# Kernel optimization log

Measured on AMD Instinct MI355X. Metric: run time of the kernel, lower is better.

Reference implementation:

```python
import jax, jax.numpy as jnp
import numpy as np

B, N, PLANE, H, W = 2, 6, 64, 48, 48
HIDP = 64
PS = 3
RATES = 3


def conv2d(x, w, b, pad, dil=1):
    # x: [BN, Cin, H, W], w: [Cout, Cin, kh, kw]
    out = jax.lax.conv_general_dilated(
        x, w, window_strides=(1, 1),
        padding=[(pad, pad), (pad, pad)],
        rhs_dilation=(dil, dil),
        dimension_numbers=('NCHW', 'OIHW', 'NCHW'))
    return out + b[None, :, None, None]


def avgpool3(x):
    bn, c, h, w = x.shape
    return x.reshape(bn, c, h // PS, PS, w // PS, PS).mean(axis=(3, 5))


def setup_inputs() -> dict:
    key = jax.random.key(0)
    ks = jax.random.split(key, 20)
    s = 0.05
    hid_pa = PLANE * 3  # 192, hidden width of MultiFieldConv2d
    d = {
        'x': jax.random.normal(ks[0], (B, N, PLANE, H, W), jnp.float32),
        # patch_aggr: 3 dilated convs (rates 1..3), k=3, plane -> plane*3
        'pa_w1': jax.random.normal(ks[1], (hid_pa, PLANE, 3, 3)) * s,
        'pa_b1': jnp.zeros((hid_pa,)),
        'pa_w2': jax.random.normal(ks[2], (hid_pa, PLANE, 3, 3)) * s,
        'pa_b2': jnp.zeros((hid_pa,)),
        'pa_w3': jax.random.normal(ks[3], (hid_pa, PLANE, 3, 3)) * s,
        'pa_b3': jnp.zeros((hid_pa,)),
        # convert: 1x1 (hid_pa*rates -> 3*hidp), relu, 1x1 (3*hidp -> 3*hidp)
        'pa_cw1': jax.random.normal(ks[4], (3 * HIDP, hid_pa * RATES, 1, 1)) * s,
        'pa_cb1': jnp.zeros((3 * HIDP,)),
        'pa_cw2': jax.random.normal(ks[5], (3 * HIDP, 3 * HIDP, 1, 1)) * s,
        'pa_cb2': jnp.zeros((3 * HIDP,)),
        # to_kv conv: k=3 pad=1, hidp -> hidp
        'kv_w': jax.random.normal(ks[6], (HIDP, HIDP, 3, 3)) * s,
        'kv_b': jnp.zeros((HIDP,)),
        # to_out: 1x1 hidp->plane, relu, 1x1 plane->plane, relu
        'out_w1': jax.random.normal(ks[7], (PLANE, HIDP, 1, 1)) * s,
        'out_b1': jnp.zeros((PLANE,)),
        'out_w2': jax.random.normal(ks[8], (PLANE, PLANE, 1, 1)) * s,
        'out_b2': jnp.zeros((PLANE,)),
        'scales': jnp.ones((N,)),
    }
    return d


def reference(x, pa_w1, pa_b1, pa_w2, pa_b2, pa_w3, pa_b3,
              pa_cw1, pa_cb1, pa_cw2, pa_cb2,
              kv_w, kv_b, out_w1, out_b1, out_w2, out_b2, scales):
    b, n, c, h, w = x.shape
    scale = HIDP ** (-0.5)
    xf = x.reshape(b * n, c, h, w)

    # MultiFieldConv2d: dilated convs (same spatial size for odd k), concat, 1x1 convert
    u = jnp.concatenate([
        conv2d(xf, pa_w1, pa_b1, pad=1, dil=1),
        conv2d(xf, pa_w2, pa_b2, pad=2, dil=2),
        conv2d(xf, pa_w3, pa_b3, pad=3, dil=3),
    ], axis=1)
    qkv = conv2d(jax.nn.relu(conv2d(u, pa_cw1, pa_cb1, 0)), pa_cw2, pa_cb2, 0)
    qkv = jax.nn.relu(qkv)  # F.relu(patch_aggr(x))
    xq, xk, xv = jnp.split(qkv, 3, axis=1)  # each [BN, hidp, H, W]

    def to_kv(t):
        return avgpool3(jax.nn.relu(conv2d(t, kv_w, kv_b, pad=PS // 2)))

    k_ = to_kv(xk)                       # [BN, hidp, H/3, W/3]
    v_ = to_kv(xv) * (1.0 / PS ** 2)

    hw_kv = k_.shape[2] * k_.shape[3]
    Qs = xq.reshape(b, n, HIDP, h * w).transpose(0, 1, 3, 2)   # b n g d
    Ks = k_.reshape(b, n, HIDP, hw_kv).transpose(0, 1, 3, 2)   # b m k d
    Vs = v_.reshape(b, n, HIDP, hw_kv).transpose(0, 1, 3, 2)

    # Leave-one-out sigmoid attention: sum_{j != i} sigmoid(q_i k_j^T * scale) @ v_j
    # Computed as full sum minus the self (j == i) term (exact same math).
    A_all = jax.nn.sigmoid(jnp.einsum('bngd,bmkd->bngmk', Qs, Ks) * scale)
    out_all = jnp.einsum('bngmk,bmkd->bngd', A_all, Vs)
    A_self = jax.nn.sigmoid(jnp.einsum('bngd,bnkd->bngk', Qs, Ks) * scale)
    out_self = jnp.einsum('bngk,bnkd->bngd', A_self, Vs)
    attn_out = out_all - out_self                               # [b, n, HW, hidp]

    res = attn_out.transpose(0, 1, 3, 2).reshape(b, n, HIDP, h, w)
    xv5 = xv.reshape(b, n, HIDP, h, w)
    res = jax.nn.relu(res + scales[None, :, None, None, None] * xv5)

    rf = res.reshape(b * n, HIDP, h, w)
    o = jax.nn.relu(conv2d(jax.nn.relu(conv2d(rf, out_w1, out_b1, 0)), out_w2, out_b2, 0))
    return o.reshape(b, n, c, h, w)
```

## Files before the change

kernel.cpp:

```cpp
#include <hip/hip_runtime.h>
#include <hip/hip_bf16.h>
#include <math.h>

#define BB 2
#define NVIEW 6
#define BN 12
#define CIN 64
#define HH 48
#define WW 48
#define PP (HH*WW)
#define OC 192
#define HPA 192
#define HIDP 64
#define KHW 16
#define PK 256
#define PADW 54
#define PADA (PADW*PADW)
#define NTOT (BN*PP)
#define K1 1728
#define KVPW 50
#define KVPA (KVPW*KVPW)

typedef __attribute__((ext_vector_type(8))) short bf16x8;
typedef __attribute__((ext_vector_type(4))) float f32x4;

#define OFF_WEFFB 0
#define SZ_WEFFB_FL (OC*K1/2)
#define OFF_BEFF (OFF_WEFFB + SZ_WEFFB_FL)
#define SZ_BEFF 256
#define OFF_CW2B (OFF_BEFF + SZ_BEFF)
#define SZ_CW2B_FL (OC*OC/2)
#define OFF_WKVB (OFF_CW2B + SZ_CW2B_FL)
#define SZ_WKVB_FL (64*576/2)
#define OFF_PADXT (OFF_WKVB + SZ_WKVB_FL)
#define SZ_PADXT_FL (BN*PADA*64/2)
#define OFF_QB16 (OFF_PADXT + SZ_PADXT_FL)
#define SZ_QB16_FL (BN*PP*64/2)
#define OFF_KB16 (OFF_QB16 + SZ_QB16_FL)
#define SZ_KB16_FL (BN*PK*64/2)
#define OFF_VB16T (OFF_KB16 + SZ_KB16_FL)
#define SZ_VB16T_FL (BN*64*PK/2)
#define OFF_KVPAD (OFF_VB16T + SZ_VB16T_FL)
#define SZ_KVPAD_FL (BN*2*KVPA*64/2)
#define OFF_CONVB (OFF_KVPAD + SZ_KVPAD_FL)
#define SZ_CONVB_FL (BN*2*PP*64/2)
#define OFF_W1SW (OFF_CONVB + SZ_CONVB_FL)
#define SZ_WSW_FL 2048
#define OFF_W2SW (OFF_W1SW + SZ_WSW_FL)
#define OFF_ATTNP (OFF_W2SW + SZ_WSW_FL)
#define SZ_ATTNP (BN*PP*HIDP)
#define OFF_XVB16 (OFF_ATTNP + 2*SZ_ATTNP)
#define SZ_XVB16_FL (BN*PP*64/2)

__device__ __forceinline__ void load_lds16(const void* g, void* l) {
    __builtin_amdgcn_global_load_lds(
        (const __attribute__((address_space(1))) unsigned int*)g,
        (__attribute__((address_space(3))) unsigned int*)l, 16, 0, 0);
}

__device__ __forceinline__ unsigned short f2bu(float f) {
    __hip_bfloat16 h = __float2bfloat16(f);
    return *(unsigned short*)&h;
}

__device__ __forceinline__ float bu2f(unsigned short h) {
    unsigned int u = ((unsigned int)h) << 16;
    return *(float*)&u;
}

__global__ void k_fold(const float* __restrict__ cw1, const float* __restrict__ cb1,
                       const float* __restrict__ w1, const float* __restrict__ b1,
                       const float* __restrict__ w2, const float* __restrict__ b2,
                       const float* __restrict__ w3, const float* __restrict__ b3,
                       __hip_bfloat16* __restrict__ weffb, float* __restrict__ beff) {
    int r = blockIdx.x / OC;
    int o = blockIdx.x % OC;
    int t = threadIdx.x;
    int ic = t / 9, tap = t % 9;
    const float* w = (r==0) ? w1 : (r==1) ? w2 : w3;
    float acc = 0.f;
    for (int c = 0; c < HPA; ++c)
        acc += cw1[o*(HPA*3) + r*HPA + c] * w[c*(CIN*9) + t];
    weffb[(size_t)o*K1 + r*576 + tap*64 + ic] = __float2bfloat16(acc);
    if (r == 0 && t == 0) {
        float bacc = cb1[o];
        for (int rr = 0; rr < 3; ++rr) {
            const float* bb = (rr==0)?b1:(rr==1)?b2:b3;
            for (int c = 0; c < HPA; ++c)
                bacc += cw1[o*(HPA*3) + rr*HPA + c] * bb[c];
        }
        beff[o] = bacc;
    }
}

__global__ void k_wprep(const float* __restrict__ kvw, const float* __restrict__ cw2,
                        const float* __restrict__ w1, const float* __restrict__ w2,
                        __hip_bfloat16* __restrict__ wkvb, __hip_bfloat16* __restrict__ cw2b,
                        __hip_bfloat16* __restrict__ w1sw, __hip_bfloat16* __restrict__ w2sw) {
    int idx = blockIdx.x*256 + threadIdx.x;
    if (idx < 36864) {
        int oc = idx / 576, rest = idx % 576;
        int tap = rest / 64, ic = rest % 64;
        wkvb[idx] = __float2bfloat16(kvw[(oc*64 + ic)*9 + tap]);
    } else if (idx < 73728) {
        int i = idx - 36864;
        cw2b[i] = __float2bfloat16(cw2[i]);
    } else if (idx < 81920) {
        int i = idx - 73728;
        const float* w = (i < 4096) ? w1 : w2;
        __hip_bfloat16* dst = (i < 4096) ? w1sw : w2sw;
        int j = i & 4095;
        int oc = j >> 6, s = (j >> 3) & 7, e = j & 7;
        int k = ((s ^ (oc & 7)) << 3) + e;
        dst[j] = __float2bfloat16(w[oc*64 + k]);
    }
}

__global__ void k_padxT(const float* __restrict__ x, __hip_bfloat16* __restrict__ padxT) {
    int idx = blockIdx.x*256 + threadIdx.x;
    if (idx >= BN*PADA) return;
    int spos = idx % PADA; int bn = idx / PADA;
    int sy = spos / PADW, sx = spos % PADW;
    __hip_bfloat16* dst = padxT + (size_t)idx*64;
    if (sy >= 3 && sy < 51 && sx >= 3 && sx < 51) {
        const float* src = x + (size_t)bn*CIN*PP + (sy-3)*WW + (sx-3);
        #pragma unroll 8
        for (int ic = 0; ic < 64; ++ic) dst[ic] = __float2bfloat16(src[ic*PP]);
    } else {
        #pragma unroll 8
        for (int ic = 0; ic < 64; ++ic) dst[ic] = __float2bfloat16(0.f);
    }
}

__global__ void k_zero(__hip_bfloat16* __restrict__ kvpad) {
    size_t idx = ((size_t)blockIdx.x*256 + threadIdx.x)*8;
    bf16x8 z = (bf16x8){0,0,0,0,0,0,0,0};
    *(bf16x8*)(kvpad + idx) = z;
}

__global__ __launch_bounds__(512) void k_mfc(const __hip_bfloat16* __restrict__ wA,
        const __hip_bfloat16* __restrict__ pxT, const __hip_bfloat16* __restrict__ cw2b,
        const float* __restrict__ beff, const float* __restrict__ cb2,
        __hip_bfloat16* __restrict__ xvb16, __hip_bfloat16* __restrict__ qb16,
        __hip_bfloat16* __restrict__ kvpad) {
    __shared__ __align__(16) char smem[58368];
    int tid = threadIdx.x;
    int wid = tid >> 6, lane = tid & 63;
    int bn = blockIdx.x / 18;
    int pb = (blockIdx.x % 18) * 128;
    int sgr = ((lane&7) ^ (lane>>3)) * 8;
    int wr = wid >> 1, wc = wid & 1;
    int l7 = lane & 7, lh = lane >> 4, rrow = lane & 15, gcol = lane >> 4;

    size_t gbase[5];
    #pragma unroll
    for (int s2 = 0; s2 < 5; ++s2) {
        int seg = wid*5 + s2;
        if (seg < 24) {
            int row = seg*8 + (lane>>3);
            gbase[s2] = (size_t)row*K1 + sgr;
        } else {
            int p = pb + (seg-24)*8 + (lane>>3);
            int py = p / WW, px = p % WW;
            gbase[s2] = ((size_t)bn*PADA + (py+3)*PADW + (px+3))*64 + sgr;
        }
    }

    f32x4 acc1[3][4];
    #pragma unroll
    for (int m = 0; m < 3; ++m)
        #pragma unroll
        for (int nf = 0; nf < 4; ++nf) acc1[m][nf] = (f32x4){0.f,0.f,0.f,0.f};

    for (int kt = 0; kt < 27; ++kt) {
        int r_ = kt / 9, tap = kt - r_*9;
        int doff = (r_+1)*((tap/3 - 1)*PADW + (tap%3 - 1));
        __syncthreads();
        #pragma unroll
        for (int s2 = 0; s2 < 5; ++s2) {
            int seg = wid*5 + s2;
            const __hip_bfloat16* g = (seg < 24) ? wA + gbase[s2] + kt*64
                                                 : pxT + gbase[s2] + (size_t)doff*64;
            load_lds16(g, smem + seg*1024);
        }
        __syncthreads();
        bf16x8 a[3][2], b[4][2];
        #pragma unroll
        for (int kk = 0; kk < 2; ++kk) {
            int gof = ((kk*4 + lh) ^ l7) << 4;
            #pragma unroll
            for (int m = 0; m < 3; ++m)
                a[m][kk] = *(const bf16x8*)(smem + (wr*48 + m*16 + rrow)*128 + gof);
            #pragma unroll
            for (int nf = 0; nf < 4; ++nf)
                b[nf][kk] = *(const bf16x8*)(smem + 24576 + (wc*64 + nf*16 + rrow)*128 + gof);
        }
        #pragma unroll
        for (int kk = 0; kk < 2; ++kk)
            #pragma unroll
            for (int m = 0; m < 3; ++m)
                #pragma unroll
                for (int nf = 0; nf < 4; ++nf)
                    acc1[m][nf] = __builtin_amdgcn_mfma_f32_16x16x32_bf16(
                        a[m][kk], b[nf][kk], acc1[m][nf], 0, 0, 0);
    }

    f32x4 acc2[3][4];
    #pragma unroll
    for (int m = 0; m < 3; ++m)
        #pragma unroll
        for (int nf = 0; nf < 4; ++nf) acc2[m][nf] = (f32x4){0.f,0.f,0.f,0.f};

    for (int kt2 = 0; kt2 < 3; ++kt2) {
        __syncthreads();
        #pragma unroll
        for (int s2 = 0; s2 < 3; ++s2) {
            int seg = wid*3 + s2;
            int row = seg*8 + (lane>>3);
            load_lds16(cw2b + (size_t)row*OC + kt2*64 + sgr, smem + seg*1024);
        }
        #pragma unroll
        for (int m = 0; m < 3; ++m) {
            int oc16 = wr*48 + m*16;
            if ((oc16 >> 6) == kt2) {
                int oc0 = oc16 + gcol*4;
                float4 bz = *(const float4*)&beff[oc0];
                int cb = (oc0 - kt2*64)*2;
                #pragma unroll
                for (int nf = 0; nf < 4; ++nf) {
                    int px = wc*64 + nf*16 + rrow;
                    ushort4 hv;
                    hv.x = f2bu(fmaxf(acc1[m][nf][0] + bz.x, 0.f));
                    hv.y = f2bu(fmaxf(acc1[m][nf][1] + bz.y, 0.f));
                    hv.z = f2bu(fmaxf(acc1[m][nf][2] + bz.z, 0.f));
                    hv.w = f2bu(fmaxf(acc1[m][nf][3] + bz.w, 0.f));
                    *(ushort4*)(smem + 40960 + px*136 + cb) = hv;
                }
            }
        }
        __syncthreads();
        #pragma unroll
        for (int kk = 0; kk < 2; ++kk) {
            int gofA = ((kk*4 + lh) ^ l7) << 4;
            int gofB = (kk*4 + lh) << 4;
            bf16x8 a2[3], b2[4];
            #pragma unroll
            for (int m2 = 0; m2 < 3; ++m2)
                a2[m2] = *(const bf16x8*)(smem + (wr*48 + m2*16 + rrow)*128 + gofA);
            #pragma unroll
            for (int nf = 0; nf < 4; ++nf)
                b2[nf] = *(const bf16x8*)(smem + 40960 + (wc*64 + nf*16 + rrow)*136 + gofB);
            #pragma unroll
            for (int m2 = 0; m2 < 3; ++m2)
                #pragma unroll
                for (int nf = 0; nf < 4; ++nf)
                    acc2[m2][nf] = __builtin_amdgcn_mfma_f32_16x16x32_bf16(
                        a2[m2], b2[nf], acc2[m2][nf], 0, 0, 0);
        }
    }

    #pragma unroll
    for (int m2 = 0; m2 < 3; ++m2) {
        int oc16 = wr*48 + m2*16;
        int sec = oc16 >> 6;
        int oc0 = oc16 + gcol*4;
        float4 cz = *(const float4*)&cb2[oc0];
        #pragma unroll
        for (int nf = 0; nf < 4; ++nf) {
            int px = wc*64 + nf*16 + rrow;
            int p = pb + px;
            ushort4 bv;
            bv.x = f2bu(fmaxf(acc2[m2][nf][0] + cz.x, 0.f));
            bv.y = f2bu(fmaxf(acc2[m2][nf][1] + cz.y, 0.f));
            bv.z = f2bu(fmaxf(acc2[m2][nf][2] + cz.z, 0.f));
            bv.w = f2bu(fmaxf(acc2[m2][nf][3] + cz.w, 0.f));
            if (sec == 0) {
                *(ushort4*)&qb16[((size_t)bn*PP + p)*64 + oc0] = bv;
            } else {
                int kv = sec - 1;
                int py = p / WW, pxx = p % WW;
                int d = oc0 - (sec << 6);
                *(ushort4*)&kvpad[((size_t)(bn*2+kv)*KVPA + (py+1)*KVPW + pxx+1)*64 + d] = bv;
                if (kv == 1)
                    *(ushort4*)&xvb16[((size_t)bn*PP + p)*64 + d] = bv;
            }
        }
    }
}

__global__ __launch_bounds__(256) void k_kvgemm(const __hip_bfloat16* __restrict__ wA,
        const __hip_bfloat16* __restrict__ kvpad, const float* __restrict__ kvb,
        __hip_bfloat16* __restrict__ convb) {
    __shared__ __align__(16) char smem[24576];
    int tid = threadIdx.x;
    int wid = tid >> 6, lane = tid & 63;
    int tileN = blockIdx.x * 128;
    int bn2 = tileN / PP, p0 = tileN % PP;
    int sgr = ((lane&7) ^ (lane>>3)) * 8;

    size_t gbase[6];
    #pragma unroll
    for (int s2 = 0; s2 < 6; ++s2) {
        int seg = wid*6 + s2;
        if (seg < 8) {
            int row = seg*8 + (lane>>3);
            gbase[s2] = (size_t)row*576 + sgr;
        } else {
            int p = p0 + (seg-8)*8 + (lane>>3);
            int py = p / WW, px = p % WW;
            gbase[s2] = ((size_t)bn2*KVPA + (py+1)*KVPW + px+1)*64 + sgr;
        }
    }
    int wr = wid >> 1, wc = wid & 1;
    int l7 = lane & 7, lh = lane >> 4;
    int arowb[2], browb[4];
    #pragma unroll
    for (int m = 0; m < 2; ++m)
        arowb[m] = (wr*32 + m*16 + (lane&15))*128;
    #pragma unroll
    for (int nf = 0; nf < 4; ++nf)
        browb[nf] = 8192 + (wc*64 + nf*16 + (lane&15))*128;

    f32x4 acc[2][4];
    #pragma unroll
    for (int m = 0; m < 2; ++m)
        #pragma unroll
        for (int nf = 0; nf < 4; ++nf) acc[m][nf] = (f32x4){0.f,0.f,0.f,0.f};

    for (int kt = 0; kt < 9; ++kt) {
        int dy = kt/3 - 1, dx = kt%3 - 1;
        int doff = dy*KVPW + dx;
        __syncthreads();
        #pragma unroll
        for (int s2 = 0; s2 < 6; ++s2) {
            int seg = wid*6 + s2;
            const __hip_bfloat16* g = (seg < 8) ? wA + gbase[s2] + kt*64
                                                : kvpad + gbase[s2] + (size_t)doff*64;
            load_lds16(g, smem + seg*1024);
        }
        __syncthreads();
        bf16x8 a[2][2], b[4][2];
        #pragma unroll
        for (int kk = 0; kk < 2; ++kk) {
            int gof = ((kk*4 + lh) ^ l7) << 4;
            #pragma unroll
            for (int m = 0; m < 2; ++m)
                a[m][kk] = *(const bf16x8*)(smem + arowb[m] + gof);
            #pragma unroll
            for (int nf = 0; nf < 4; ++nf)
                b[nf][kk] = *(const bf16x8*)(smem + browb[nf] + gof);
        }
        #pragma unroll
        for (int kk = 0; kk < 2; ++kk)
            #pragma unroll
            for (int m = 0; m < 2; ++m)
                #pragma unroll
                for (int nf = 0; nf < 4; ++nf)
                    acc[m][nf] = __builtin_amdgcn_mfma_f32_16x16x32_bf16(
                        a[m][kk], b[nf][kk], acc[m][nf], 0, 0, 0);
    }
    #pragma unroll
    for (int m = 0; m < 2; ++m) {
        int rbase = wr*32 + m*16 + (lane>>4)*4;
        float4 bz = *(const float4*)&kvb[rbase];
        #pragma unroll
        for (int nf = 0; nf < 4; ++nf) {
            int col = p0 + wc*64 + nf*16 + (lane&15);
            ushort4 cv;
            cv.x = f2bu(fmaxf(acc[m][nf][0] + bz.x, 0.f));
            cv.y = f2bu(fmaxf(acc[m][nf][1] + bz.y, 0.f));
            cv.z = f2bu(fmaxf(acc[m][nf][2] + bz.z, 0.f));
            cv.w = f2bu(fmaxf(acc[m][nf][3] + bz.w, 0.f));
            *(ushort4*)&convb[((size_t)bn2*PP + col)*64 + rbase] = cv;
        }
    }
}

__global__ __launch_bounds__(256) void k_pool(const __hip_bfloat16* __restrict__ convb,
        __hip_bfloat16* __restrict__ kbufb, __hip_bfloat16* __restrict__ vbufT) {
    int idx = blockIdx.x*256 + threadIdx.x;
    int dg = idx % 8; idx /= 8;
    int pp = idx % PK; idx /= PK;
    int bn2 = idx;
    int kv = bn2 & 1, bn = bn2 >> 1;
    int qy = pp / KHW, qx = pp % KHW;
    float s[8] = {0,0,0,0,0,0,0,0};
    const __hip_bfloat16* base = convb + (size_t)bn2*PP*64 + dg*8;
    #pragma unroll
    for (int sy = 0; sy < 3; ++sy)
        #pragma unroll
        for (int sx = 0; sx < 3; ++sx) {
            union { bf16x8 v; unsigned short h[8]; } c;
            c.v = *(const bf16x8*)(base + ((size_t)(qy*3+sy)*WW + qx*3+sx)*64);
            #pragma unroll
            for (int j = 0; j < 8; ++j) s[j] += bu2f(c.h[j]);
        }
    if (kv == 0) {
        union { ushort4 u[2]; unsigned short h[8]; } cv;
        #pragma unroll
        for (int j = 0; j < 8; ++j) cv.h[j] = f2bu(s[j] * (1.f/9.f));
        ushort4* dst = (ushort4*)(kbufb + ((size_t)bn*PK + pp)*64 + dg*8);
        dst[0] = cv.u[0]; dst[1] = cv.u[1];
    } else {
        #pragma unroll
        for (int j = 0; j < 8; ++j)
            vbufT[((size_t)bn*64 + dg*8 + j)*PK + pp] = __float2bfloat16(s[j]*(1.f/81.f));
    }
}

__global__ __launch_bounds__(256) void k_attn3(const __hip_bfloat16* __restrict__ qb16,
        const __hip_bfloat16* __restrict__ kbufb, const __hip_bfloat16* __restrict__ vbufT,
        float* __restrict__ attnp) {
    __shared__ __align__(16) char smem[32768];
    char* Qs = smem;
    char* Ks = smem + 8192;
    char* Vs = smem + 16384;
    char* Ps = smem + 24576;
    int tid = threadIdx.x;
    int wid = tid >> 6, lane = tid & 63;
    int bid = blockIdx.x;
    int ks = bid & 1; bid >>= 1;
    int qt = bid % 36; int bn = bid / 36;
    int b = bn / NVIEW, n = bn % NVIEW;
    int p0 = qt*64;

    {
        const char* gq = (const char*)(qb16 + ((size_t)bn*PP + p0)*64);
        #pragma unroll
        for (int i = 0; i < 2; ++i) {
            int s = wid*2 + i;
            int lin = s*1024 + lane*16;
            int r = lin >> 7, c = (lin >> 4) & 7;
            int gof = (r<<7) + ((c ^ (r&7)) << 4);
            load_lds16(gq + gof, Qs + s*1024);
        }
    }
    int arow = wid*16 + (lane&15);
    int brow = lane&15;
    int gcol = lane>>4;
    int vrow = tid >> 2;
    int vc2 = (tid & 3) * 2;

    f32x4 oacc[4];
    #pragma unroll
    for (int i = 0; i < 4; ++i) oacc[i] = (f32x4){0,0,0,0};

    for (int mi = 0; mi < NVIEW-1; ++mi) {
        int m = mi + (mi >= n ? 1 : 0);
        int bnk = b*NVIEW + m;
        const char* gk = (const char*)(kbufb + (size_t)bnk*PK*64);
        const __hip_bfloat16* gv = vbufT + (size_t)bnk*64*PK;
        for (int kc = ks*2; kc < ks*2+2; ++kc) {
            __syncthreads();
            #pragma unroll
            for (int i = 0; i < 2; ++i) {
                int s = wid*2 + i;
                int lin = s*1024 + lane*16;
                int r = lin >> 7, c = (lin >> 4) & 7;
                int gof = (r<<7) + ((c ^ (r&7)) << 4);
                load_lds16(gk + (size_t)kc*8192 + gof, Ks + s*1024);
            }
            {
                const __hip_bfloat16* src = gv + vrow*PK + kc*64 + vc2*8;
                bf16x8 v0 = *(const bf16x8*)src;
                bf16x8 v1 = *(const bf16x8*)(src+8);
                *(bf16x8*)(Vs + vrow*128 + ((vc2 ^ (vrow&7))<<4)) = v0;
                *(bf16x8*)(Vs + vrow*128 + (((vc2+1) ^ (vrow&7))<<4)) = v1;
            }
            __syncthreads();
            f32x4 sacc[4];
            #pragma unroll
            for (int i = 0; i < 4; ++i) sacc[i] = (f32x4){0,0,0,0};
            #pragma unroll
            for (int kk = 0; kk < 2; ++kk) {
                int g = kk*4 + gcol;
                bf16x8 af = *(const bf16x8*)(Ks + arow*128 + ((g ^ (arow&7))<<4));
                #pragma unroll
                for (int nf = 0; nf < 4; ++nf) {
                    int q = nf*16 + brow;
                    bf16x8 bq = *(const bf16x8*)(Qs + q*128 + ((g ^ (q&7))<<4));
                    sacc[nf] = __builtin_amdgcn_mfma_f32_16x16x32_bf16(af, bq, sacc[nf], 0,0,0);
                }
            }
            {
                int kbase = wid*16 + gcol*4;
                #pragma unroll
                for (int nf = 0; nf < 4; ++nf) {
                    int q = nf*16 + brow;
                    ushort4 pu;
                    float e0 = __expf(-sacc[nf][0]*0.125f);
                    float e1 = __expf(-sacc[nf][1]*0.125f);
                    float e2 = __expf(-sacc[nf][2]*0.125f);
                    float e3 = __expf(-sacc[nf][3]*0.125f);
                    pu.x = f2bu(__builtin_amdgcn_rcpf(1.f+e0));
                    pu.y = f2bu(__builtin_amdgcn_rcpf(1.f+e1));
                    pu.z = f2bu(__builtin_amdgcn_rcpf(1.f+e2));
                    pu.w = f2bu(__builtin_amdgcn_rcpf(1.f+e3));
                    *(ushort4*)(Ps + q*128 + (((kbase>>3) ^ (q&7))<<4) + (kbase&7)*2) = pu;
                }
            }
            __syncthreads();
            #pragma unroll
            for (int kk = 0; kk < 2; ++kk) {
                int g = kk*4 + gcol;
                int qr = wid*16 + brow;
                bf16x8 pf = *(const bf16x8*)(Ps + qr*128 + ((g ^ (qr&7))<<4));
                #pragma unroll
                for (int nf = 0; nf < 4; ++nf) {
                    int d = nf*16 + brow;
                    bf16x8 vf = *(const bf16x8*)(Vs + d*128 + ((g ^ (d&7))<<4));
                    oacc[nf] = __builtin_amdgcn_mfma_f32_16x16x32_bf16(pf, vf, oacc[nf], 0,0,0);
                }
            }
        }
    }
    float* ab = attnp + (size_t)ks*SZ_ATTNP + ((size_t)bn*PP + p0)*64;
    #pragma unroll
    for (int nf = 0; nf < 4; ++nf) {
        #pragma unroll
        for (int r = 0; r < 4; ++r) {
            int q = wid*16 + gcol*4 + r;
            int d = nf*16 + brow;
            ab[(size_t)q*64 + d] = oacc[nf][r];
        }
    }
}

__global__ __launch_bounds__(256) void k_out2(const float* __restrict__ attnp,
        const __hip_bfloat16* __restrict__ xvb16, const float* __restrict__ scales,
        const __hip_bfloat16* __restrict__ w1sw, const __hip_bfloat16* __restrict__ w2sw,
        const float* __restrict__ b1, const float* __restrict__ b2,
        float* __restrict__ out) {
    __shared__ __align__(16) char smem[49152];
    char* W1s = smem;
    char* W2s = smem + 8192;
    char* Rs  = smem + 16384;
    char* Ts  = smem + 32768;
    int tid = threadIdx.x;
    int wid = tid >> 6, lane = tid & 63;
    int pix0 = blockIdx.x * 128;
    int bn = pix0 / PP;
    int pb = pix0 - bn*PP;
    float sc = scales[bn % NVIEW];

    #pragma unroll
    for (int i = 0; i < 4; ++i) {
        int seg = wid*4 + i;
        const char* src = (seg < 8) ? (const char*)w1sw + seg*1024
                                    : (const char*)w2sw + (seg-8)*1024;
        load_lds16(src + lane*16, smem + seg*1024);
    }
    {
        int p = tid >> 1, d0 = (tid & 1) * 32;
        int P = pix0 + p;
        const float* a0 = attnp + (size_t)P*64 + d0;
        const float* a1 = a0 + SZ_ATTNP;
        const __hip_bfloat16* xv = xvb16 + (size_t)P*64 + d0;
        #pragma unroll
        for (int j = 0; j < 4; ++j) {
            float4 u0 = *(const float4*)(a0 + j*8);
            float4 u1 = *(const float4*)(a0 + j*8 + 4);
            float4 v0 = *(const float4*)(a1 + j*8);
            float4 v1 = *(const float4*)(a1 + j*8 + 4);
            union { bf16x8 v; unsigned short h[8]; } xu;
            xu.v = *(const bf16x8*)(xv + j*8);
            union { bf16x8 v; unsigned short h[8]; } rv;
            rv.h[0] = f2bu(fmaxf(u0.x + v0.x + sc*bu2f(xu.h[0]), 0.f));
            rv.h[1] = f2bu(fmaxf(u0.y + v0.y + sc*bu2f(xu.h[1]), 0.f));
            rv.h[2] = f2bu(fmaxf(u0.z + v0.z + sc*bu2f(xu.h[2]), 0.f));
            rv.h[3] = f2bu(fmaxf(u0.w + v0.w + sc*bu2f(xu.h[3]), 0.f));
            rv.h[4] = f2bu(fmaxf(u1.x + v1.x + sc*bu2f(xu.h[4]), 0.f));
            rv.h[5] = f2bu(fmaxf(u1.y + v1.y + sc*bu2f(xu.h[5]), 0.f));
            rv.h[6] = f2bu(fmaxf(u1.z + v1.z + sc*bu2f(xu.h[6]), 0.f));
            rv.h[7] = f2bu(fmaxf(u1.w + v1.w + sc*bu2f(xu.h[7]), 0.f));
            int g = (d0 >> 3) + j;
            *(bf16x8*)(Rs + p*128 + ((g ^ (p&7)) << 4)) = rv.v;
        }
    }
    __syncthreads();

    int wr = wid >> 1, wc = wid & 1;
    int rrow = lane & 15, gcol = lane >> 4;
    f32x4 acc1[2][4];
    #pragma unroll
    for (int m = 0; m < 2; ++m)
        #pragma unroll
        for (int nf = 0; nf < 4; ++nf) acc1[m][nf] = (f32x4){0,0,0,0};
    #pragma unroll
    for (int kk = 0; kk < 2; ++kk) {
        int g = kk*4 + gcol;
        #pragma unroll
        for (int m = 0; m < 2; ++m) {
            int oc = wr*32 + m*16 + rrow;
            bf16x8 af = *(const bf16x8*)(W1s + oc*128 + ((g ^ (oc&7)) << 4));
            #pragma unroll
            for (int nf = 0; nf < 4; ++nf) {
                int px = wc*64 + nf*16 + rrow;
                bf16x8 bf = *(const bf16x8*)(Rs + px*128 + ((g ^ (px&7)) << 4));
                acc1[m][nf] = __builtin_amdgcn_mfma_f32_16x16x32_bf16(af, bf, acc1[m][nf], 0,0,0);
            }
        }
    }
    #pragma unroll
    for (int m = 0; m < 2; ++m) {
        int oc0 = wr*32 + m*16 + gcol*4;
        float4 bz = *(const float4*)&b1[oc0];
        #pragma unroll
        for (int nf = 0; nf < 4; ++nf) {
            int px = wc*64 + nf*16 + rrow;
            ushort4 tv;
            tv.x = f2bu(fmaxf(acc1[m][nf][0] + bz.x, 0.f));
            tv.y = f2bu(fmaxf(acc1[m][nf][1] + bz.y, 0.f));
            tv.z = f2bu(fmaxf(acc1[m][nf][2] + bz.z, 0.f));
            tv.w = f2bu(fmaxf(acc1[m][nf][3] + bz.w, 0.f));
            *(ushort4*)(Ts + px*128 + (((oc0>>3) ^ (px&7)) << 4) + (oc0&7)*2) = tv;
        }
    }
    __syncthreads();
    f32x4 acc2[2][4];
    #pragma unroll
    for (int m = 0; m < 2; ++m)
        #pragma unroll
        for (int nf = 0; nf < 4; ++nf) acc2[m][nf] = (f32x4){0,0,0,0};
    #pragma unroll
    for (int kk = 0; kk < 2; ++kk) {
        int g = kk*4 + gcol;
        #pragma unroll
        for (int m = 0; m < 2; ++m) {
            int oc = wr*32 + m*16 + rrow;
            bf16x8 af = *(const bf16x8*)(W2s + oc*128 + ((g ^ (oc&7)) << 4));
            #pragma unroll
            for (int nf = 0; nf < 4; ++nf) {
                int px = wc*64 + nf*16 + rrow;
                bf16x8 bf = *(const bf16x8*)(Ts + px*128 + ((g ^ (px&7)) << 4));
                acc2[m][nf] = __builtin_amdgcn_mfma_f32_16x16x32_bf16(af, bf, acc2[m][nf], 0,0,0);
            }
        }
    }
    #pragma unroll
    for (int m = 0; m < 2; ++m) {
        int oc0 = wr*32 + m*16 + gcol*4;
        float4 bz = *(const float4*)&b2[oc0];
        #pragma unroll
        for (int nf = 0; nf < 4; ++nf) {
            int px = wc*64 + nf*16 + rrow;
            float* dst = out + ((size_t)bn*64 + oc0)*PP + pb + px;
            dst[0*PP] = fmaxf(acc2[m][nf][0] + bz.x, 0.f);
            dst[1*PP] = fmaxf(acc2[m][nf][1] + bz.y, 0.f);
            dst[2*PP] = fmaxf(acc2[m][nf][2] + bz.z, 0.f);
            dst[3*PP] = fmaxf(acc2[m][nf][3] + bz.w, 0.f);
        }
    }
}

extern "C" void kernel_launch(void* const* d_in, const int* in_sizes, int n_in,
                              void* d_out, int out_size, void* d_ws, size_t ws_size,
                              hipStream_t stream) {
    (void)in_sizes; (void)n_in; (void)out_size; (void)ws_size;
    const float* x      = (const float*)d_in[0];
    const float* pa_w1  = (const float*)d_in[1];
    const float* pa_b1  = (const float*)d_in[2];
    const float* pa_w2  = (const float*)d_in[3];
    const float* pa_b2  = (const float*)d_in[4];
    const float* pa_w3  = (const float*)d_in[5];
    const float* pa_b3  = (const float*)d_in[6];
    const float* pa_cw1 = (const float*)d_in[7];
    const float* pa_cb1 = (const float*)d_in[8];
    const float* pa_cw2 = (const float*)d_in[9];
    const float* pa_cb2 = (const float*)d_in[10];
    const float* kv_w   = (const float*)d_in[11];
    const float* kv_b   = (const float*)d_in[12];
    const float* out_w1 = (const float*)d_in[13];
    const float* out_b1 = (const float*)d_in[14];
    const float* out_w2 = (const float*)d_in[15];
    const float* out_b2 = (const float*)d_in[16];
    const float* scales = (const float*)d_in[17];
    float* out = (float*)d_out;
    float* ws  = (float*)d_ws;

    __hip_bfloat16* weffb = (__hip_bfloat16*)(ws + OFF_WEFFB);
    float* beff = ws + OFF_BEFF;
    __hip_bfloat16* cw2b  = (__hip_bfloat16*)(ws + OFF_CW2B);
    __hip_bfloat16* wkvb  = (__hip_bfloat16*)(ws + OFF_WKVB);
    __hip_bfloat16* padxT = (__hip_bfloat16*)(ws + OFF_PADXT);
    __hip_bfloat16* qb16  = (__hip_bfloat16*)(ws + OFF_QB16);
    __hip_bfloat16* kbufb = (__hip_bfloat16*)(ws + OFF_KB16);
    __hip_bfloat16* vbufT = (__hip_bfloat16*)(ws + OFF_VB16T);
    __hip_bfloat16* kvpad = (__hip_bfloat16*)(ws + OFF_KVPAD);
    __hip_bfloat16* convb = (__hip_bfloat16*)(ws + OFF_CONVB);
    __hip_bfloat16* w1sw  = (__hip_bfloat16*)(ws + OFF_W1SW);
    __hip_bfloat16* w2sw  = (__hip_bfloat16*)(ws + OFF_W2SW);
    float* attnp = ws + OFF_ATTNP;
    __hip_bfloat16* xvb16 = (__hip_bfloat16*)(ws + OFF_XVB16);

    k_fold<<<3*OC, CIN*9, 0, stream>>>(pa_cw1, pa_cb1, pa_w1, pa_b1,
                                       pa_w2, pa_b2, pa_w3, pa_b3, weffb, beff);
    k_wprep<<<320, 256, 0, stream>>>(kv_w, pa_cw2, out_w1, out_w2,
                                     wkvb, cw2b, w1sw, w2sw);
    k_padxT<<<(BN*PADA+255)/256, 256, 0, stream>>>(x, padxT);
    k_zero<<<(BN*2*KVPA*64/8)/256, 256, 0, stream>>>(kvpad);
    k_mfc<<<NTOT/128, 512, 0, stream>>>(weffb, padxT, cw2b, beff, pa_cb2,
                                        xvb16, qb16, kvpad);
    k_kvgemm<<<BN*2*PP/128, 256, 0, stream>>>(wkvb, kvpad, kv_b, convb);
    k_pool<<<BN*2*PK*8/256, 256, 0, stream>>>(convb, kbufb, vbufT);
    k_attn3<<<BN*36*2, 256, 0, stream>>>(qb16, kbufb, vbufT, attnp);
    k_out2<<<NTOT/128, 256, 0, stream>>>(attnp, xvb16, scales, w1sw, w2sw,
                                         out_b1, out_b2, out);
}
```

Before: 122.8 us.

## Retile MFC GEMM to 64-pixel blocks, zero only KV halo, batch weight fold

The fused multi-field conv GEMM kernel moves from 512-thread blocks covering 128 pixels to 256-thread blocks covering 64 pixels. This doubles the grid and cuts shared memory per block, which should give more blocks per CU and better occupancy, at the cost of loading the weight tiles twice as often per pixel. The full zeroing pass over the padded KV buffer is replaced by a kernel that writes only the one-pixel halo border, since the interior is overwritten anyway. The weight-fold kernel now computes 8 output channels per thread, reusing each loaded conv weight across them and launching far fewer blocks.

```diff
diff --git a/kernel.cpp b/kernel.cpp
--- a/kernel.cpp
+++ b/kernel.cpp
@@ -73,16 +73,23 @@
                        const float* __restrict__ w2, const float* __restrict__ b2,
                        const float* __restrict__ w3, const float* __restrict__ b3,
                        __hip_bfloat16* __restrict__ weffb, float* __restrict__ beff) {
-    int r = blockIdx.x / OC;
-    int o = blockIdx.x % OC;
+    int r = blockIdx.x / 24;
+    int og = blockIdx.x % 24;
     int t = threadIdx.x;
     int ic = t / 9, tap = t % 9;
     const float* w = (r==0) ? w1 : (r==1) ? w2 : w3;
-    float acc = 0.f;
-    for (int c = 0; c < HPA; ++c)
-        acc += cw1[o*(HPA*3) + r*HPA + c] * w[c*(CIN*9) + t];
-    weffb[(size_t)o*K1 + r*576 + tap*64 + ic] = __float2bfloat16(acc);
-    if (r == 0 && t == 0) {
+    float acc[8] = {0,0,0,0,0,0,0,0};
+    for (int c = 0; c < HPA; ++c) {
+        float wv = w[c*(CIN*9) + t];
+        #pragma unroll
+        for (int j = 0; j < 8; ++j)
+            acc[j] += cw1[(og*8+j)*(HPA*3) + r*HPA + c] * wv;
+    }
+    #pragma unroll
+    for (int j = 0; j < 8; ++j)
+        weffb[(size_t)(og*8+j)*K1 + r*576 + tap*64 + ic] = __float2bfloat16(acc[j]);
+    if (r == 0 && t < 8) {
+        int o = og*8 + t;
         float bacc = cb1[o];
         for (int rr = 0; rr < 3; ++rr) {
             const float* bb = (rr==0)?b1:(rr==1)?b2:b3;
@@ -132,30 +139,38 @@
     }
 }
 
-__global__ void k_zero(__hip_bfloat16* __restrict__ kvpad) {
-    size_t idx = ((size_t)blockIdx.x*256 + threadIdx.x)*8;
+__global__ void k_halo(__hip_bfloat16* __restrict__ kvpad) {
+    int idx = blockIdx.x*256 + threadIdx.x;
+    if (idx >= 24*196) return;
+    int bn2 = idx / 196, h = idx % 196;
+    int py, px;
+    if (h < 50)       { py = 0;        px = h; }
+    else if (h < 100) { py = 49;       px = h - 50; }
+    else if (h < 148) { py = h - 99;   px = 0; }
+    else              { py = h - 147;  px = 49; }
     bf16x8 z = (bf16x8){0,0,0,0,0,0,0,0};
-    *(bf16x8*)(kvpad + idx) = z;
-}
-
-__global__ __launch_bounds__(512) void k_mfc(const __hip_bfloat16* __restrict__ wA,
+    __hip_bfloat16* dst = kvpad + ((size_t)bn2*KVPA + py*KVPW + px)*64;
+    #pragma unroll
+    for (int j = 0; j < 8; ++j) *(bf16x8*)(dst + j*8) = z;
+}
+
+__global__ __launch_bounds__(256) void k_mfc(const __hip_bfloat16* __restrict__ wA,
         const __hip_bfloat16* __restrict__ pxT, const __hip_bfloat16* __restrict__ cw2b,
         const float* __restrict__ beff, const float* __restrict__ cb2,
         __hip_bfloat16* __restrict__ xvb16, __hip_bfloat16* __restrict__ qb16,
         __hip_bfloat16* __restrict__ kvpad) {
-    __shared__ __align__(16) char smem[58368];
+    __shared__ __align__(16) char smem[41472];
     int tid = threadIdx.x;
     int wid = tid >> 6, lane = tid & 63;
-    int bn = blockIdx.x / 18;
-    int pb = (blockIdx.x % 18) * 128;
+    int bn = blockIdx.x / 36;
+    int pb = (blockIdx.x % 36) * 64;
     int sgr = ((lane&7) ^ (lane>>3)) * 8;
-    int wr = wid >> 1, wc = wid & 1;
     int l7 = lane & 7, lh = lane >> 4, rrow = lane & 15, gcol = lane >> 4;
 
-    size_t gbase[5];
-    #pragma unroll
-    for (int s2 = 0; s2 < 5; ++s2) {
-        int seg = wid*5 + s2;
+    size_t gbase[8];
+    #pragma unroll
+    for (int s2 = 0; s2 < 8; ++s2) {
+        int seg = wid*8 + s2;
         if (seg < 24) {
             int row = seg*8 + (lane>>3);
             gbase[s2] = (size_t)row*K1 + sgr;
@@ -177,8 +192,8 @@
         int doff = (r_+1)*((tap/3 - 1)*PADW + (tap%3 - 1));
         __syncthreads();
         #pragma unroll
-        for (int s2 = 0; s2 < 5; ++s2) {
-            int seg = wid*5 + s2;
+        for (int s2 = 0; s2 < 8; ++s2) {
+            int seg = wid*8 + s2;
             const __hip_bfloat16* g = (seg < 24) ? wA + gbase[s2] + kt*64
                                                  : pxT + gbase[s2] + (size_t)doff*64;
             load_lds16(g, smem + seg*1024);
@@ -190,10 +205,10 @@
             int gof = ((kk*4 + lh) ^ l7) << 4;
             #pragma unroll
             for (int m = 0; m < 3; ++m)
-                a[m][kk] = *(const bf16x8*)(smem + (wr*48 + m*16 + rrow)*128 + gof);
+                a[m][kk] = *(const bf16x8*)(smem + (wid*48 + m*16 + rrow)*128 + gof);
             #pragma unroll
             for (int nf = 0; nf < 4; ++nf)
-                b[nf][kk] = *(const bf16x8*)(smem + 24576 + (wc*64 + nf*16 + rrow)*128 + gof);
+                b[nf][kk] = *(const bf16x8*)(smem + 24576 + (nf*16 + rrow)*128 + gof);
         }
         #pragma unroll
         for (int kk = 0; kk < 2; ++kk)
@@ -214,27 +229,27 @@
     for (int kt2 = 0; kt2 < 3; ++kt2) {
         __syncthreads();
         #pragma unroll
-        for (int s2 = 0; s2 < 3; ++s2) {
-            int seg = wid*3 + s2;
+        for (int s2 = 0; s2 < 6; ++s2) {
+            int seg = wid*6 + s2;
             int row = seg*8 + (lane>>3);
             load_lds16(cw2b + (size_t)row*OC + kt2*64 + sgr, smem + seg*1024);
         }
         #pragma unroll
         for (int m = 0; m < 3; ++m) {
-            int oc16 = wr*48 + m*16;
+            int oc16 = wid*48 + m*16;
             if ((oc16 >> 6) == kt2) {
                 int oc0 = oc16 + gcol*4;
                 float4 bz = *(const float4*)&beff[oc0];
                 int cb = (oc0 - kt2*64)*2;
                 #pragma unroll
                 for (int nf = 0; nf < 4; ++nf) {
-                    int px = wc*64 + nf*16 + rrow;
+                    int px = nf*16 + rrow;
                     ushort4 hv;
                     hv.x = f2bu(fmaxf(acc1[m][nf][0] + bz.x, 0.f));
                     hv.y = f2bu(fmaxf(acc1[m][nf][1] + bz.y, 0.f));
                     hv.z = f2bu(fmaxf(acc1[m][nf][2] + bz.z, 0.f));
                     hv.w = f2bu(fmaxf(acc1[m][nf][3] + bz.w, 0.f));
-                    *(ushort4*)(smem + 40960 + px*136 + cb) = hv;
+                    *(ushort4*)(smem + 32768 + px*136 + cb) = hv;
                 }
             }
         }
@@ -246,10 +261,10 @@
             bf16x8 a2[3], b2[4];
             #pragma unroll
             for (int m2 = 0; m2 < 3; ++m2)
-                a2[m2] = *(const bf16x8*)(smem + (wr*48 + m2*16 + rrow)*128 + gofA);
+                a2[m2] = *(const bf16x8*)(smem + (wid*48 + m2*16 + rrow)*128 + gofA);
             #pragma unroll
             for (int nf = 0; nf < 4; ++nf)
-                b2[nf] = *(const bf16x8*)(smem + 40960 + (wc*64 + nf*16 + rrow)*136 + gofB);
+                b2[nf] = *(const bf16x8*)(smem + 32768 + (nf*16 + rrow)*136 + gofB);
             #pragma unroll
             for (int m2 = 0; m2 < 3; ++m2)
                 #pragma unroll
@@ -261,13 +276,13 @@
 
     #pragma unroll
     for (int m2 = 0; m2 < 3; ++m2) {
-        int oc16 = wr*48 + m2*16;
+        int oc16 = wid*48 + m2*16;
         int sec = oc16 >> 6;
         int oc0 = oc16 + gcol*4;
         float4 cz = *(const float4*)&cb2[oc0];
         #pragma unroll
         for (int nf = 0; nf < 4; ++nf) {
-            int px = wc*64 + nf*16 + rrow;
+            int px = nf*16 + rrow;
             int p = pb + px;
             ushort4 bv;
             bv.x = f2bu(fmaxf(acc2[m2][nf][0] + cz.x, 0.f));
@@ -693,14 +708,14 @@
     float* attnp = ws + OFF_ATTNP;
     __hip_bfloat16* xvb16 = (__hip_bfloat16*)(ws + OFF_XVB16);
 
-    k_fold<<<3*OC, CIN*9, 0, stream>>>(pa_cw1, pa_cb1, pa_w1, pa_b1,
+    k_fold<<<3*24, CIN*9, 0, stream>>>(pa_cw1, pa_cb1, pa_w1, pa_b1,
                                        pa_w2, pa_b2, pa_w3, pa_b3, weffb, beff);
     k_wprep<<<320, 256, 0, stream>>>(kv_w, pa_cw2, out_w1, out_w2,
                                      wkvb, cw2b, w1sw, w2sw);
     k_padxT<<<(BN*PADA+255)/256, 256, 0, stream>>>(x, padxT);
-    k_zero<<<(BN*2*KVPA*64/8)/256, 256, 0, stream>>>(kvpad);
-    k_mfc<<<NTOT/128, 512, 0, stream>>>(weffb, padxT, cw2b, beff, pa_cb2,
-                                        xvb16, qb16, kvpad);
+    k_halo<<<(24*196+255)/256, 256, 0, stream>>>(kvpad);
+    k_mfc<<<NTOT/64, 256, 0, stream>>>(weffb, padxT, cw2b, beff, pa_cb2,
+                                       xvb16, qb16, kvpad);
     k_kvgemm<<<BN*2*PP/128, 256, 0, stream>>>(wkvb, kvpad, kv_b, convb);
     k_pool<<<BN*2*PK*8/256, 256, 0, stream>>>(convb, kbufb, vbufT);
     k_attn3<<<BN*36*2, 256, 0, stream>>>(qb16, kbufb, vbufT, attnp);
```

New measurement: 137.3 us. +11.8%, slower.
